# Kernel tuning notes

Hardware: AMD Instinct MI355X
Metric: run time of the kernel (lower is better)

Reference implementation:

```python
import jax, jax.numpy as jnp
import numpy as np

B = 16384
LEN_VOCAB = 2048
IPD_VOCAB = 2048
EBDIN = 32


def setup_inputs() -> dict:
    key = jax.random.key(0)
    ks = jax.random.split(key, 11)
    return {
        "x": jax.random.randint(ks[0], (B, 1, 2), 0, LEN_VOCAB, dtype=jnp.int64)
        if jax.config.jax_enable_x64 else jax.random.randint(ks[0], (B, 1, 2), 0, LEN_VOCAB),
        "lenebdLUT": jax.random.normal(ks[1], (LEN_VOCAB, EBDIN), jnp.float32),
        "ipdebdLUT": jax.random.normal(ks[2], (IPD_VOCAB, EBDIN), jnp.float32),
        "S1": jax.random.normal(ks[3], (15, 2, 15), jnp.float32),
        "H1": jax.random.normal(ks[4], (45, 4096), jnp.float32),
        "T1": jax.random.normal(ks[5], (15, 15), jnp.float32),
        "LUT1": jax.random.normal(ks[6], (5, 4096, 32), jnp.float32),
        "S2": jax.random.normal(ks[7], (1, 2, 15), jnp.float32),
        "H2": jax.random.normal(ks[8], (15, 16), jnp.float32),
        "T2": jax.random.normal(ks[9], (1, 15), jnp.float32),
        "LUT2": jax.random.normal(ks[10], (1, 16, 32), jnp.float32),
    }


def _forward(x, lenebdLUT, ipdebdLUT, S1, H1, T1, LUT1, S2, H2, T2, LUT2):
    batch = x.shape[0]
    # embedding lookups, summed: [B,1,32] -> flatten to [B,32] (seq==1)
    e = (lenebdLUT[x[:, :, 0]] + ipdebdLUT[x[:, :, 1]]).reshape(-1, EBDIN)
    ebd = e
    # ---- newMM on first 30 features ----
    a = jnp.einsum('bcd,cdk->bck', e[:, :30].reshape(-1, 15, 2), S1)  # [B,15,15]
    a = a - T1 - 1e-4
    t = jnp.tanh(a)
    a = jax.lax.stop_gradient(jnp.sign(a) - t) + t  # straight-through sign
    a = a.reshape(-1, 5, 45)
    scores1 = jnp.einsum('bcd,dk->bck', a, H1)       # [B,5,4096]
    idx1 = jnp.argmax(scores1, axis=-1)              # [B,5]
    # one_hot(argmax) @ LUT == per-codebook gather
    x1 = LUT1[jnp.arange(5)[None, :], idx1]          # [B,5,32]
    # ---- MM_final on last 2 features ----
    b = jnp.einsum('bcd,cdk->bck', e[:, 30:32].reshape(-1, 1, 2), S2)  # [B,1,15]
    b = b - T2
    b = jnp.where(b == 0, jnp.float32(-1.0), jnp.sign(b))  # x[x==0]=-1; sign(x)
    scores2 = jnp.einsum('bcd,dk->bck', b, H2)       # [B,1,16]
    idx2 = jnp.argmax(scores2, axis=-1)              # [B,1]
    x2 = LUT2[jnp.arange(1)[None, :], idx2]          # [B,1,32]
    x2 = jnp.sum(x2, axis=1).reshape(batch, 1, 32)
    reconstruct = jnp.concatenate([x1, x2], axis=1).sum(axis=1)  # [B,32]
    return reconstruct, ebd


def reference(x, lenebdLUT, ipdebdLUT, S1, H1, T1, LUT1, S2, H2, T2, LUT2):
    return _forward(x, lenebdLUT, ipdebdLUT, S1, H1, T1, LUT1, S2, H2, T2, LUT2)
```

## Files before the change

kernel.cpp:

```cpp
#include <hip/hip_runtime.h>

#define B_TOT 16384
#define NPAIR (B_TOT*5)
#define NPT32 (NPAIR/32)
#define NKG   8
#define KTPG  16
#define KTB   9216

#define PREP_BLKS 288
#define SIGN_BLKS 320
#define EMBD_BLKS 64

typedef __attribute__((ext_vector_type(8))) short bf16x8;
typedef __attribute__((ext_vector_type(16))) float f32x16;

struct alignas(8) us4 { unsigned short x, y, z, w; };

__device__ inline unsigned short f2bf(float f) {
    unsigned u = __builtin_bit_cast(unsigned, f);
    unsigned r = u + 0x7fffu + ((u >> 16) & 1u);
    return (unsigned short)(r >> 16);
}
__device__ inline float bf2f(unsigned short b) {
    unsigned u = ((unsigned)b) << 16;
    return __builtin_bit_cast(float, u);
}
__device__ inline float max3f(float a, float b, float c) {
    return fmaxf(fmaxf(a, b), c);
}

__global__ __launch_bounds__(256) void kfront(
    const int* __restrict__ x,
    const float* __restrict__ lenLUT, const float* __restrict__ ipdLUT,
    const float* __restrict__ S1, const float* __restrict__ H1,
    const float* __restrict__ T1,
    const float* __restrict__ S2, const float* __restrict__ H2,
    const float* __restrict__ T2, const float* __restrict__ LUT2,
    float* __restrict__ out, float* __restrict__ p2vec,
    unsigned short* __restrict__ Abuf, unsigned short* __restrict__ Bbuf) {
    const int bid = blockIdx.x;
    const int tid = threadIdx.x;

    if (bid < PREP_BLKS) {
        int blk = bid * 4 + (tid >> 6);
        int kt = blk / 9, rem = blk - kt*9;
        int s = rem / 3, q = rem - s*3;
        int l = tid & 63;
        int h = l >> 5;
        int row = kt*32 + (l & 31);
        unsigned short o[8];
#pragma unroll
        for (int j = 0; j < 8; ++j) {
            int d = 16*s + 4*h + ((j < 4) ? j : (j + 4));
            float v = (d < 45) ? H1[(size_t)d*4096 + row] : 0.f;
            unsigned short bb = 0;
            for (int qq = 0; qq <= q; ++qq) { bb = f2bf(v); v -= bf2f(bb); }
            o[j] = bb;
        }
        unsigned short* dst = Abuf + (size_t)blk*512 + l*8;
        *(us4*)(dst)     = us4{o[0], o[1], o[2], o[3]};
        *(us4*)(dst + 4) = us4{o[4], o[5], o[6], o[7]};
        return;
    }

    if (bid < PREP_BLKS + SIGN_BLKS) {
        int p = (bid - PREP_BLKS) * 256 + tid;
        int b = p / 5;
        int c = p - b * 5;
        int x0 = x[2*b], x1 = x[2*b+1];
        float e[6];
        const float2* l2 = (const float2*)(lenLUT + (size_t)x0*32 + 6*c);
        const float2* i2 = (const float2*)(ipdLUT + (size_t)x1*32 + 6*c);
#pragma unroll
        for (int t = 0; t < 3; ++t) {
            float2 a = l2[t], d = i2[t];
            e[2*t]   = a.x + d.x;
            e[2*t+1] = a.y + d.y;
        }
        unsigned short sg[48];
#pragma unroll
        for (int t = 0; t < 3; ++t) {
            int c15 = 3*c + t;
#pragma unroll
            for (int k = 0; k < 15; ++k) {
                float a = e[2*t] * S1[(2*c15)*15 + k] + e[2*t+1] * S1[(2*c15+1)*15 + k];
                a = a - T1[c15*15 + k];
                a = a - 1e-4f;
                sg[t*15+k] = (a > 0.f) ? (unsigned short)0x3F80u
                           : ((a < 0.f) ? (unsigned short)0xBF80u : (unsigned short)0);
            }
        }
        sg[45] = 0; sg[46] = 0; sg[47] = 0;
        int P = p >> 5, col = p & 31;
        unsigned short* base = Bbuf + (size_t)P*1536;
#pragma unroll
        for (int s = 0; s < 3; ++s) {
            unsigned short* blk = base + s*512;
            *(us4*)(blk + col*8)          = us4{sg[16*s+0],  sg[16*s+1],  sg[16*s+2],  sg[16*s+3]};
            *(us4*)(blk + col*8 + 4)      = us4{sg[16*s+8],  sg[16*s+9],  sg[16*s+10], sg[16*s+11]};
            *(us4*)(blk + (col+32)*8)     = us4{sg[16*s+4],  sg[16*s+5],  sg[16*s+6],  sg[16*s+7]};
            *(us4*)(blk + (col+32)*8 + 4) = us4{sg[16*s+12], sg[16*s+13], sg[16*s+14], sg[16*s+15]};
        }
        return;
    }

    {
        int b = (bid - PREP_BLKS - SIGN_BLKS) * 256 + tid;
        if (b >= B_TOT) return;
        int x0 = x[2*b], x1 = x[2*b+1];
        const float4* l4 = (const float4*)(lenLUT + (size_t)x0*32);
        const float4* i4 = (const float4*)(ipdLUT + (size_t)x1*32);
        float4* o4 = (float4*)(out + (size_t)B_TOT*32 + (size_t)b*32);
        float e30 = 0.f, e31 = 0.f;
#pragma unroll
        for (int j = 0; j < 8; ++j) {
            float4 a = l4[j], c = i4[j];
            float4 sv; sv.x=a.x+c.x; sv.y=a.y+c.y; sv.z=a.z+c.z; sv.w=a.w+c.w;
            o4[j] = sv;
            if (j == 7) { e30 = sv.z; e31 = sv.w; }
        }
        float sb[15];
#pragma unroll
        for (int k = 0; k < 15; ++k) {
            float bb = e30 * S2[k] + e31 * S2[15 + k];
            bb = bb - T2[k];
            sb[k] = (bb > 0.f) ? 1.f : -1.f;
        }
        float best = -3.4e38f; int bi = 0;
#pragma unroll
        for (int k2 = 0; k2 < 16; ++k2) {
            float sc = 0.f;
#pragma unroll
            for (int d = 0; d < 15; ++d) sc = fmaf(sb[d], H2[d*16 + k2], sc);
            if (sc > best) { best = sc; bi = k2; }
        }
        const float4* lr = (const float4*)(LUT2 + (size_t)bi*32);
        float4* pv = (float4*)(p2vec + (size_t)b*32);
#pragma unroll
        for (int j = 0; j < 8; ++j) pv[j] = lr[j];
    }
}

__global__ __launch_bounds__(256, 2) void k2m(
    const unsigned short* __restrict__ Abuf,
    const unsigned short* __restrict__ Bbuf,
    float* __restrict__ pval, int* __restrict__ pidx) {
    const int bid = blockIdx.x;
    const int kg = bid & 7;
    const int pg = bid >> 3;
    const int tid = threadIdx.x;
    const int w = tid >> 6, l = tid & 63;
    const int pt0 = pg*8 + w*2;

    bf16x8 Bf[2][3];
#pragma unroll
    for (int i = 0; i < 2; ++i)
#pragma unroll
        for (int s = 0; s < 3; ++s)
            Bf[i][s] = *(const bf16x8*)(Bbuf + ((size_t)(pt0+i)*3 + s)*512 + l*8);

    float bv16[2][16];
    float V[2] = {-3.4e38f, -3.4e38f};
    int bkt[2] = {0, 0};
#pragma unroll
    for (int i = 0; i < 2; ++i)
#pragma unroll
        for (int r = 0; r < 16; ++r) bv16[i][r] = -3.4e38f;

    const char* Asrc = (const char*)Abuf + (size_t)kg*KTPG*KTB + (size_t)l*16;

    f32x16 zf;
#pragma unroll
    for (int r = 0; r < 16; ++r) zf[r] = 0.f;

#pragma unroll 2
    for (int ktl = 0; ktl < 16; ++ktl) {
        const char* ab = Asrc + (size_t)ktl*KTB;
        bf16x8 A[9];
#pragma unroll
        for (int f = 0; f < 9; ++f)
            A[f] = *(const bf16x8*)(ab + f*1024);

        f32x16 acc0, acc1;
        acc0 = __builtin_amdgcn_mfma_f32_32x32x16_bf16(A[0], Bf[0][0], zf, 0, 0, 0);
        acc1 = __builtin_amdgcn_mfma_f32_32x32x16_bf16(A[0], Bf[1][0], zf, 0, 0, 0);
#pragma unroll
        for (int s = 0; s < 3; ++s)
#pragma unroll
            for (int q = 0; q < 3; ++q) {
                if (s == 0 && q == 0) continue;
                const int f = s*3 + q;
                acc0 = __builtin_amdgcn_mfma_f32_32x32x16_bf16(A[f], Bf[0][s], acc0, 0, 0, 0);
                acc1 = __builtin_amdgcn_mfma_f32_32x32x16_bf16(A[f], Bf[1][s], acc1, 0, 0, 0);
            }
#pragma unroll
        for (int i = 0; i < 2; ++i) {
            const f32x16& a = (i == 0) ? acc0 : acc1;
            float m0 = max3f(a[0],  a[1],  a[2]);
            float m1 = max3f(a[3],  a[4],  a[5]);
            float m2 = max3f(a[6],  a[7],  a[8]);
            float m3 = max3f(a[9],  a[10], a[11]);
            float m4 = max3f(a[12], a[13], a[14]);
            float m5 = max3f(m0, m1, a[15]);
            float m6 = max3f(m2, m3, m4);
            float t  = fmaxf(m5, m6);
            bkt[i] = (t > V[i]) ? ktl : bkt[i];
            V[i] = fmaxf(V[i], t);
#pragma unroll
            for (int r = 0; r < 16; ++r)
                bv16[i][r] = fmaxf(bv16[i][r], a[r]);
        }
    }

    const int h = l >> 5;
#pragma unroll
    for (int i = 0; i < 2; ++i) {
        int rb = 0;
#pragma unroll
        for (int r = 15; r >= 0; --r)
            rb = (bv16[i][r] == V[i]) ? r : rb;
        int kk = kg*512 + bkt[i]*32 + (rb & 3) + ((rb >> 2) << 3) + (h << 2);
        float v = V[i];
        float ov = __shfl_xor(v, 32);
        int   ok = __shfl_xor(kk, 32);
        if (ov > v || (ov == v && ok < kk)) { v = ov; kk = ok; }
        if (l < 32) {
            int pair = (pt0 + i)*32 + l;
            pval[(size_t)pair*NKG + kg] = v;
            pidx[(size_t)pair*NKG + kg] = kk;
        }
    }
}

__global__ __launch_bounds__(256) void k3_final(
    const float* __restrict__ pval, const int* __restrict__ pidx,
    const float* __restrict__ LUT1, const float* __restrict__ p2vec,
    float* __restrict__ out) {
    int t = blockIdx.x * 256 + threadIdx.x;
    int b = t >> 3, j = t & 7;
    if (b >= B_TOT) return;
    float4 r = ((const float4*)(p2vec + (size_t)b*32))[j];
#pragma unroll
    for (int c = 0; c < 5; ++c) {
        size_t pair = (size_t)b*5 + c;
        const float4* pv4 = (const float4*)(pval + pair*NKG);
        const int4*   pi4 = (const int4*)(pidx + pair*NKG);
        float4 v0 = pv4[0], v1 = pv4[1];
        int4   i0 = pi4[0], i1 = pi4[1];
        float vv[8] = {v0.x, v0.y, v0.z, v0.w, v1.x, v1.y, v1.z, v1.w};
        int   ii[8] = {i0.x, i0.y, i0.z, i0.w, i1.x, i1.y, i1.z, i1.w};
        float bvv = vv[0]; int bk = ii[0];
#pragma unroll
        for (int q = 1; q < 8; ++q) {
            if (vv[q] > bvv) { bvv = vv[q]; bk = ii[q]; }
        }
        float4 tl = ((const float4*)(LUT1 + ((size_t)c*4096 + bk)*32))[j];
        r.x += tl.x; r.y += tl.y; r.z += tl.z; r.w += tl.w;
    }
    ((float4*)(out + (size_t)b*32))[j] = r;
}

extern "C" void kernel_launch(void* const* d_in, const int* in_sizes, int n_in,
                              void* d_out, int out_size, void* d_ws, size_t ws_size,
                              hipStream_t stream) {
    const int*   x      = (const int*)d_in[0];
    const float* lenLUT = (const float*)d_in[1];
    const float* ipdLUT = (const float*)d_in[2];
    const float* S1     = (const float*)d_in[3];
    const float* H1     = (const float*)d_in[4];
    const float* T1     = (const float*)d_in[5];
    const float* LUT1   = (const float*)d_in[6];
    const float* S2     = (const float*)d_in[7];
    const float* H2     = (const float*)d_in[8];
    const float* T2     = (const float*)d_in[9];
    const float* LUT2   = (const float*)d_in[10];
    float* out = (float*)d_out;

    char* ws = (char*)d_ws;
    unsigned short* Abuf = (unsigned short*)ws;
    size_t off = (size_t)1152*1024;
    unsigned short* Bbuf = (unsigned short*)(ws + off);
    off += (size_t)NPT32*1536*2;
    float* p2vec = (float*)(ws + off);
    off += (size_t)B_TOT*32*4;
    float* pval  = (float*)(ws + off);
    off += (size_t)NPAIR*NKG*4;
    int*   pidx  = (int*)(ws + off);

    kfront<<<dim3(PREP_BLKS + SIGN_BLKS + EMBD_BLKS), dim3(256), 0, stream>>>(
        x, lenLUT, ipdLUT, S1, H1, T1, S2, H2, T2, LUT2, out, p2vec, Abuf, Bbuf);
    k2m<<<dim3(NPT32), dim3(256), 0, stream>>>(Abuf, Bbuf, pval, pidx);
    k3_final<<<dim3(B_TOT*8/256), dim3(256), 0, stream>>>(
        pval, pidx, LUT1, p2vec, out);
}
```

Baseline: 102.5 us.

## Stage A tiles through an LDS ring with async global_load_lds prefetch

The k2m GEMM/argmax kernel no longer has each wave read its A tile straight from global memory. The four waves now cooperatively copy each tile into a 4-slot LDS ring using global_load_lds, keeping three tiles in flight, with explicit vmcnt waits and a barrier before each compute step. This removes the four-fold redundant global reads of the same tile and overlaps memory latency with MFMA work. It also raises launch bounds to 3 blocks per CU and wraps the MFMA chain in s_setprio. The cost is 36 KB of LDS per block, a block-wide barrier every iteration, and hand-counted vmcnt values that must stay consistent with the load count.

```diff
diff --git a/kernel.cpp b/kernel.cpp
--- a/kernel.cpp
+++ b/kernel.cpp
@@ -141,7 +141,15 @@
     }
 }
 
-__global__ __launch_bounds__(256, 2) void k2m(
+__device__ __forceinline__ void waitvm6() { asm volatile("s_waitcnt vmcnt(6)" ::: "memory"); }
+__device__ __forceinline__ void waitvm3() { asm volatile("s_waitcnt vmcnt(3)" ::: "memory"); }
+__device__ __forceinline__ void waitvm0() { asm volatile("s_waitcnt vmcnt(0)" ::: "memory"); }
+__device__ __forceinline__ void barrier_fenced() {
+    asm volatile("s_barrier" ::: "memory");
+    __builtin_amdgcn_sched_barrier(0);
+}
+
+__global__ __launch_bounds__(256, 3) void k2m(
     const unsigned short* __restrict__ Abuf,
     const unsigned short* __restrict__ Bbuf,
     float* __restrict__ pval, int* __restrict__ pidx) {
@@ -152,12 +160,15 @@
     const int w = tid >> 6, l = tid & 63;
     const int pt0 = pg*8 + w*2;
 
+    __shared__ __align__(16) char lds[4][KTB];
+
     bf16x8 Bf[2][3];
 #pragma unroll
     for (int i = 0; i < 2; ++i)
 #pragma unroll
         for (int s = 0; s < 3; ++s)
             Bf[i][s] = *(const bf16x8*)(Bbuf + ((size_t)(pt0+i)*3 + s)*512 + l*8);
+    waitvm0();
 
     float bv16[2][16];
     float V[2] = {-3.4e38f, -3.4e38f};
@@ -167,21 +178,37 @@
 #pragma unroll
         for (int r = 0; r < 16; ++r) bv16[i][r] = -3.4e38f;
 
-    const char* Asrc = (const char*)Abuf + (size_t)kg*KTPG*KTB + (size_t)l*16;
+    const char* Asrc = (const char*)Abuf + (size_t)kg*KTPG*KTB;
+
+#define STAGE(t) do {                                                          \
+        const char* sb_ = Asrc + (size_t)(t)*KTB + w*2304;                     \
+        char* db_ = &lds[(t) & 3][w*2304];                                     \
+        __builtin_amdgcn_global_load_lds(                                      \
+            (const __attribute__((address_space(1))) unsigned int*)(sb_ + l*16),          \
+            (__attribute__((address_space(3))) unsigned int*)(db_ + l*16), 16, 0, 0);     \
+        __builtin_amdgcn_global_load_lds(                                      \
+            (const __attribute__((address_space(1))) unsigned int*)(sb_ + 1024 + l*16),   \
+            (__attribute__((address_space(3))) unsigned int*)(db_ + 1024 + l*16), 16, 0, 0); \
+        __builtin_amdgcn_global_load_lds(                                      \
+            (const __attribute__((address_space(1))) unsigned int*)(sb_ + 2048 + l*4),    \
+            (__attribute__((address_space(3))) unsigned int*)(db_ + 2048 + l*4), 4, 0, 0);   \
+    } while (0)
+
+    STAGE(0); STAGE(1); STAGE(2);
 
     f32x16 zf;
 #pragma unroll
     for (int r = 0; r < 16; ++r) zf[r] = 0.f;
 
-#pragma unroll 2
-    for (int ktl = 0; ktl < 16; ++ktl) {
-        const char* ab = Asrc + (size_t)ktl*KTB;
+    auto compute = [&](int ktl) {
+        const char* ab = &lds[ktl & 3][l*16];
         bf16x8 A[9];
 #pragma unroll
         for (int f = 0; f < 9; ++f)
             A[f] = *(const bf16x8*)(ab + f*1024);
 
         f32x16 acc0, acc1;
+        __builtin_amdgcn_s_setprio(1);
         acc0 = __builtin_amdgcn_mfma_f32_32x32x16_bf16(A[0], Bf[0][0], zf, 0, 0, 0);
         acc1 = __builtin_amdgcn_mfma_f32_32x32x16_bf16(A[0], Bf[1][0], zf, 0, 0, 0);
 #pragma unroll
@@ -193,6 +220,7 @@
                 acc0 = __builtin_amdgcn_mfma_f32_32x32x16_bf16(A[f], Bf[0][s], acc0, 0, 0, 0);
                 acc1 = __builtin_amdgcn_mfma_f32_32x32x16_bf16(A[f], Bf[1][s], acc1, 0, 0, 0);
             }
+        __builtin_amdgcn_s_setprio(0);
 #pragma unroll
         for (int i = 0; i < 2; ++i) {
             const f32x16& a = (i == 0) ? acc0 : acc1;
@@ -210,7 +238,17 @@
             for (int r = 0; r < 16; ++r)
                 bv16[i][r] = fmaxf(bv16[i][r], a[r]);
         }
-    }
+    };
+
+    for (int ktl = 0; ktl < 14; ++ktl) {
+        waitvm6();
+        barrier_fenced();
+        if (ktl < 13) STAGE(ktl + 3);
+        compute(ktl);
+    }
+    waitvm3();  barrier_fenced();  compute(14);
+    waitvm0();  barrier_fenced();  compute(15);
+#undef STAGE
 
     const int h = l >> 5;
 #pragma unroll
```

New measurement: 108.3 us. +5.7%, slower.
